# Kernel optimization log

Measured on AMD Instinct MI355X. Metric: run time of the kernel, lower is better.

Reference implementation:

```python
import jax, jax.numpy as jnp
import numpy as np

# dimensions
B, NQ, D, H, L, KT, KF = 4, 8192, 256, 8, 4, 2, 2
K = KT * KF
DH = D // H
SPATIAL = np.array([[64, 64], [32, 32], [16, 16], [8, 8]], dtype=np.int32)  # (H_l, W_l)
_sizes = SPATIAL[:, 0] * SPATIAL[:, 1]
LSI = np.concatenate([[0], np.cumsum(_sizes)[:-1]]).astype(np.int32)
NV = int(_sizes.sum())


def setup_inputs() -> dict:
    key = jax.random.key(0)
    ks = jax.random.split(key, 12)
    s = 0.02  # small weight scale keeps tanh in linear region like the zero-init original
    # biases per _reset_parameters: +-0.5 grid for offsets, level-specialization for level_weights
    b_time = jnp.asarray(np.tile(np.linspace(-0.5, 0.5, KT), H * L).astype(np.float32))
    b_freq = jnp.asarray(np.tile(np.linspace(-0.5, 0.5, KF).astype(np.float32), H * L))
    lvl_bias = np.zeros((H, L), dtype=np.float32)
    hpl = max(1, H // L)
    for lvl in range(L):
        lvl_bias[lvl * hpl:min(lvl * hpl + hpl, H), lvl] = 1.0
    return dict(
        query=jax.random.normal(ks[0], (B, NQ, D), jnp.float32),
        reference_points=jax.random.uniform(ks[1], (B, NQ, L, 2), jnp.float32),
        value=jax.random.normal(ks[2], (B, NV, D), jnp.float32),
        spatial_shapes=jnp.asarray(SPATIAL),
        level_start_index=jnp.asarray(LSI),
        W_time=jax.random.normal(ks[3], (D, H * L * KT), jnp.float32) * s,
        b_time=b_time,
        W_freq=jax.random.normal(ks[4], (D, H * L * KF), jnp.float32) * s,
        b_freq=b_freq,
        W_lvl=jax.random.normal(ks[5], (D, H * L), jnp.float32) * s,
        b_lvl=jnp.asarray(lvl_bias.reshape(-1)),
        W_pt=jax.random.normal(ks[6], (D, H * L * K), jnp.float32) * s,
        b_pt=jnp.zeros((H * L * K,), jnp.float32),
        W_v=jax.random.normal(ks[7], (D, D), jnp.float32) * (1.0 / np.sqrt(D)),
        b_v=jnp.zeros((D,), jnp.float32),
        W_o=jax.random.normal(ks[8], (D, D), jnp.float32) * (1.0 / np.sqrt(D)),
        b_o=jnp.zeros((D,), jnp.float32),
    )


def _bilinear(vlev, gx, gy, Hl, Wl):
    # vlev: [B,H,Hl*Wl,DH]; gx,gy: [B,H,NQ,K] normalized grid coords in [-1,1]
    # F.grid_sample(align_corners=False, padding_mode='zeros') semantics
    x = (gx + 1.0) * (Wl * 0.5) - 0.5
    y = (gy + 1.0) * (Hl * 0.5) - 0.5
    x0 = jnp.floor(x)
    y0 = jnp.floor(y)
    wx1 = x - x0
    wy1 = y - y0
    x0i = x0.astype(jnp.int32)
    y0i = y0.astype(jnp.int32)

    def gather(xi, yi, w):
        valid = (xi >= 0) & (xi < Wl) & (yi >= 0) & (yi < Hl)
        idx = jnp.clip(yi, 0, Hl - 1) * Wl + jnp.clip(xi, 0, Wl - 1)
        b, h, nq, k = idx.shape
        v = jnp.take_along_axis(vlev, idx.reshape(b, h, nq * k)[..., None], axis=2)
        v = v.reshape(b, h, nq, k, DH)
        return v * (w * valid)[..., None]

    return (gather(x0i, y0i, (1.0 - wx1) * (1.0 - wy1))
            + gather(x0i + 1, y0i, wx1 * (1.0 - wy1))
            + gather(x0i, y0i + 1, (1.0 - wx1) * wy1)
            + gather(x0i + 1, y0i + 1, wx1 * wy1))


def _forward(query, reference_points, value, W_time, b_time, W_freq, b_freq,
             W_lvl, b_lvl, W_pt, b_pt, W_v, b_v, W_o, b_o,
             spatial_shapes, level_start_index):
    ss = np.asarray(spatial_shapes)
    lsi = np.asarray(level_start_index)
    # predicted separable offsets (offset_scale = 1.0)
    t_off = jnp.tanh(query @ W_time + b_time).reshape(B, NQ, H, L, KT)
    f_off = jnp.tanh(query @ W_freq + b_freq).reshape(B, NQ, H, L, KF)
    # square grid: outer product of time (x) and freq (y) offsets -> K = KT*KF points
    off = jnp.stack([
        jnp.broadcast_to(t_off[..., :, None], (B, NQ, H, L, KT, KF)),
        jnp.broadcast_to(f_off[..., None, :], (B, NQ, H, L, KT, KF)),
    ], axis=-1).reshape(B, NQ, H, L, K, 2)
    # normalizer: (W_l, H_l) per level
    norm = jnp.stack([spatial_shapes[:, 1], spatial_shapes[:, 0]], axis=-1).astype(jnp.float32)
    loc = reference_points[:, :, None, :, None, :] + off / norm[None, None, None, :, None, :]
    loc = jnp.clip(loc, 0.0, 1.0)
    grid = 2.0 * loc - 1.0  # [B,NQ,H,L,K,2], last dim = (x, y)
    # attention weights: softmax over levels times softmax over points
    lw = jax.nn.softmax((query @ W_lvl + b_lvl).reshape(B, NQ, H, L), axis=-1)
    pw = jax.nn.softmax((query @ W_pt + b_pt).reshape(B, NQ, H, L, K), axis=-1)
    attn = lw[..., None] * pw  # [B,NQ,H,L,K]
    v = (value @ W_v + b_v).reshape(B, NV, H, DH)
    out = jnp.zeros((B, NQ, H, DH), jnp.float32)
    for lid in range(L):
        Hl, Wl = int(ss[lid, 0]), int(ss[lid, 1])
        start = int(lsi[lid])
        vlev = v[:, start:start + Hl * Wl].transpose(0, 2, 1, 3)  # [B,H,S_l,DH]
        gx = grid[:, :, :, lid, :, 0].transpose(0, 2, 1, 3)  # [B,H,NQ,K]
        gy = grid[:, :, :, lid, :, 1].transpose(0, 2, 1, 3)
        sampled = _bilinear(vlev, gx, gy, Hl, Wl)  # [B,H,NQ,K,DH]
        a = attn[:, :, :, lid, :].transpose(0, 2, 1, 3)  # [B,H,NQ,K]
        out = out + jnp.einsum('bhqkd,bhqk->bqhd', sampled, a)
    out = out.reshape(B, NQ, D)
    return out @ W_o + b_o


def reference(query, reference_points, value, spatial_shapes, level_start_index,
              W_time, b_time, W_freq, b_freq, W_lvl, b_lvl, W_pt, b_pt,
              W_v, b_v, W_o, b_o):
    return _forward(query, reference_points, value, W_time, b_time, W_freq, b_freq,
                    W_lvl, b_lvl, W_pt, b_pt, W_v, b_v, W_o, b_o,
                    spatial_shapes, level_start_index)
```

## Files before the change

### kernel.cpp

```cpp
#include <hip/hip_runtime.h>
#include <math.h>

#define B_  4
#define NQ_ 8192
#define D_  256
#define H_  8
#define L_  4
#define K_  4
#define DH_ 32
#define NV_ 5440

#define SLAB_ 5936

typedef short bf16x8 __attribute__((ext_vector_type(8)));
typedef float f32x4  __attribute__((ext_vector_type(4)));
typedef unsigned short u16x8 __attribute__((ext_vector_type(8)));

__device__ __forceinline__ ushort f2bf(float f) {
    union { float f; unsigned u; } v; v.f = f;
    return (ushort)((v.u + 0x7FFF + ((v.u >> 16) & 1)) >> 16);
}
__device__ __forceinline__ float bf2f(ushort u) {
    union { unsigned u; float f; } v; v.u = ((unsigned)u) << 16;
    return v.f;
}

__global__ __launch_bounds__(256) void k_zero(uint4* __restrict__ p) {
    p[(size_t)blockIdx.x * 256 + threadIdx.x] = make_uint4(0, 0, 0, 0);
}

__global__ __launch_bounds__(256) void k_cvta(const float* __restrict__ in,
                                              ushort* __restrict__ out) {
    const size_t base = ((size_t)blockIdx.x * 256 + threadIdx.x) * 8;
    const float4 a = *(const float4*)(in + base);
    const float4 b = *(const float4*)(in + base + 4);
    u16x8 u;
    u[0] = f2bf(a.x); u[1] = f2bf(a.y); u[2] = f2bf(a.z); u[3] = f2bf(a.w);
    u[4] = f2bf(b.x); u[5] = f2bf(b.y); u[6] = f2bf(b.z); u[7] = f2bf(b.w);
    *(u16x8*)(out + base) = u;
}

__global__ __launch_bounds__(256) void k_cvtw(const float* __restrict__ in,
                                              ushort* __restrict__ out) {
    const int n = blockIdx.x, k = threadIdx.x;
    out[n * 256 + k] = f2bf(in[k * 256 + n]);
}

__global__ __launch_bounds__(256) void k_cvtwq(const float* __restrict__ Wt,
                                               const float* __restrict__ Wf,
                                               const float* __restrict__ Wlv,
                                               const float* __restrict__ Wp,
                                               ushort* __restrict__ out) {
    const int n = blockIdx.x, k = threadIdx.x;
    float v;
    if (n < 64)       v = Wt[k * 64 + n];
    else if (n < 128) v = Wf[k * 64 + (n - 64)];
    else if (n < 160) v = Wlv[k * 32 + (n - 128)];
    else              v = Wp[k * 128 + (n - 160)];
    out[n * 256 + k] = f2bf(v);
}

template<int NT, int MODE, int AF32>
__global__ __launch_bounds__(256) void k_gemm(const void* __restrict__ Ap,
                                              const ushort* __restrict__ Bt,
                                              const float* __restrict__ bias,
                                              void* __restrict__ Cp) {
    constexpr int NFN = NT / 32;
    __shared__ ushort As[128 * 32];
    __shared__ ushort Bs[NT * 32];
    const int m0   = blockIdx.x * 128;
    const int n0   = blockIdx.y * NT;
    const int t    = threadIdx.x;
    const int w    = t >> 6;
    const int lane = t & 63;
    const int wm   = (w >> 1) * 64;
    const int wn   = (w & 1) * (NT / 2);
    const int lm   = lane & 15;
    const int quad = lane >> 4;

    f32x4 acc[4][NFN];
    #pragma unroll
    for (int i = 0; i < 4; ++i)
        #pragma unroll
        for (int j = 0; j < NFN; ++j)
            acc[i][j] = (f32x4)(0.f);

    for (int kc = 0; kc < 256; kc += 32) {
        __syncthreads();
        if (AF32) {
            const float* A = (const float*)Ap;
            #pragma unroll
            for (int i = 0; i < 4; ++i) {
                const int c   = t + i * 256;
                const int row = c >> 3, ko = (c & 7) * 4;
                const float4 v = *(const float4*)&A[(size_t)(m0 + row) * 256 + kc + ko];
                ushort4 u; u.x = f2bf(v.x); u.y = f2bf(v.y); u.z = f2bf(v.z); u.w = f2bf(v.w);
                *(ushort4*)&As[row * 32 + ko] = u;
            }
        } else {
            const ushort* A = (const ushort*)Ap;
            #pragma unroll
            for (int i = 0; i < 2; ++i) {
                const int c   = t + i * 256;
                const int row = c >> 2, ko = (c & 3) * 8;
                *(u16x8*)&As[row * 32 + ko] =
                    *(const u16x8*)&A[(size_t)(m0 + row) * 256 + kc + ko];
            }
        }
        #pragma unroll
        for (int i = 0; i < 2; ++i) {
            const int c = t + i * 256;
            if (NT == 128 || c < NT * 4) {
                const int row = c >> 2, ko = (c & 3) * 8;
                *(u16x8*)&Bs[row * 32 + ko] =
                    *(const u16x8*)&Bt[(size_t)(n0 + row) * 256 + kc + ko];
            }
        }
        __syncthreads();

        bf16x8 af[4], bfr[NFN];
        #pragma unroll
        for (int mf = 0; mf < 4; ++mf)
            af[mf] = *(const bf16x8*)&As[(wm + mf * 16 + lm) * 32 + quad * 8];
        #pragma unroll
        for (int nf = 0; nf < NFN; ++nf)
            bfr[nf] = *(const bf16x8*)&Bs[(wn + nf * 16 + lm) * 32 + quad * 8];
        #pragma unroll
        for (int mf = 0; mf < 4; ++mf)
            #pragma unroll
            for (int nf = 0; nf < NFN; ++nf)
                acc[mf][nf] = __builtin_amdgcn_mfma_f32_16x16x32_bf16(
                    af[mf], bfr[nf], acc[mf][nf], 0, 0, 0);
    }

    #pragma unroll
    for (int mf = 0; mf < 4; ++mf) {
        #pragma unroll
        for (int nf = 0; nf < NFN; ++nf) {
            const f32x4 a = acc[mf][nf];
            const int col   = n0 + wn + nf * 16 + lm;
            const int rbase = m0 + wm + mf * 16 + quad * 4;
            #pragma unroll
            for (int r = 0; r < 4; ++r) {
                const int row = rbase + r;
                const float v = a[r];
                if (MODE == 0) {
                    ((float*)Cp)[(size_t)row * 256 + col] = v + bias[col];
                } else if (MODE == 1) {
                    const int b = row / NV_, s = row - b * NV_;
                    const int h = col >> 5, dh = col & 31;
                    const int l = (s >= 5376) ? 3 : (s >= 5120) ? 2 : (s >= 4096) ? 1 : 0;
                    const int lsi_[4] = {0, 4096, 5120, 5376};
                    const int po_[4]  = {0, 4356, 5512, 5836};
                    const int o  = s - lsi_[l];
                    const int Wl = 64 >> l;
                    const int y  = o >> (6 - l);
                    const int x  = o & (Wl - 1);
                    const int prow = po_[l] + (y + 1) * (Wl + 2) + (x + 1);
                    ((ushort*)Cp)[(((size_t)(b * H_ + h)) * SLAB_ + prow) * 32 + dh] =
                        f2bf(v + bias[col]);
                } else {
                    ((float*)Cp)[(size_t)row * 288 + col] = v;
                }
            }
        }
    }
}

__global__ __launch_bounds__(256) void k_epi(const float* __restrict__ logits,
                                             const float* __restrict__ refpts,
                                             const float* __restrict__ bt,
                                             const float* __restrict__ bfq,
                                             const float* __restrict__ blv,
                                             const float* __restrict__ bp,
                                             float* __restrict__ params) {
    const int item = blockIdx.x * 256 + threadIdx.x;
    const int qg = item >> 5;
    const int hl = item & 31;
    const int h = hl >> 2, l = hl & 3;
    const float* lgr = logits + (size_t)qg * 288;

    const float tA = tanhf(lgr[hl * 2 + 0] + bt[hl * 2 + 0]);
    const float tB = tanhf(lgr[hl * 2 + 1] + bt[hl * 2 + 1]);
    const float fA = tanhf(lgr[64 + hl * 2 + 0] + bfq[hl * 2 + 0]);
    const float fB = tanhf(lgr[64 + hl * 2 + 1] + bfq[hl * 2 + 1]);

    const float l0 = lgr[128 + h * 4 + 0] + blv[h * 4 + 0];
    const float l1 = lgr[128 + h * 4 + 1] + blv[h * 4 + 1];
    const float l2 = lgr[128 + h * 4 + 2] + blv[h * 4 + 2];
    const float l3 = lgr[128 + h * 4 + 3] + blv[h * 4 + 3];
    const float lm = fmaxf(fmaxf(l0, l1), fmaxf(l2, l3));
    const float e0 = __expf(l0 - lm), e1 = __expf(l1 - lm);
    const float e2 = __expf(l2 - lm), e3 = __expf(l3 - lm);
    const float lsum = e0 + e1 + e2 + e3;
    const float lwv = ((l == 0) ? e0 : (l == 1) ? e1 : (l == 2) ? e2 : e3) / lsum;

    const float p0 = lgr[160 + hl * 4 + 0] + bp[hl * 4 + 0];
    const float p1 = lgr[160 + hl * 4 + 1] + bp[hl * 4 + 1];
    const float p2 = lgr[160 + hl * 4 + 2] + bp[hl * 4 + 2];
    const float p3 = lgr[160 + hl * 4 + 3] + bp[hl * 4 + 3];
    const float pmx = fmaxf(fmaxf(p0, p1), fmaxf(p2, p3));
    const float q0e = __expf(p0 - pmx), q1e = __expf(p1 - pmx);
    const float q2e = __expf(p2 - pmx), q3e = __expf(p3 - pmx);
    const float inv = lwv / (q0e + q1e + q2e + q3e);

    const float rx = refpts[((size_t)qg * L_ + l) * 2 + 0];
    const float ry = refpts[((size_t)qg * L_ + l) * 2 + 1];
    const float Wlf = (float)(64 >> l);
    const float Hlf = (float)(64 >> l);
    const float xA = fminf(fmaxf(rx + tA / Wlf, 0.f), 1.f) * Wlf - 0.5f;
    const float xB = fminf(fmaxf(rx + tB / Wlf, 0.f), 1.f) * Wlf - 0.5f;
    const float yA = fminf(fmaxf(ry + fA / Hlf, 0.f), 1.f) * Hlf - 0.5f;
    const float yB = fminf(fmaxf(ry + fB / Hlf, 0.f), 1.f) * Hlf - 0.5f;

    float* pp = params + (size_t)qg * 256 + hl * 8;
    pp[0] = q0e * inv; pp[1] = q1e * inv; pp[2] = q2e * inv; pp[3] = q3e * inv;
    pp[4] = xA; pp[5] = xB; pp[6] = yA; pp[7] = yB;
}

__global__ __launch_bounds__(256) void k_sample(const ushort* __restrict__ vperm,
                                                const float* __restrict__ params,
                                                ushort* __restrict__ mid) {
    __shared__ float pm[8][264];
    const int b   = blockIdx.y;
    const int q0  = blockIdx.x * 8;
    const int t   = threadIdx.x;
    const int qs  = t >> 6;
    const int sub = t & 63;
    const int h   = sub >> 3;
    const int dh4 = sub & 7;

    for (int i = t; i < 8 * 256; i += 256) {
        const int q = i >> 8, c = i & 255;
        pm[q][(c >> 5) * 33 + (c & 31)] = params[((size_t)(b * NQ_ + q0 + q)) * 256 + c];
    }
    __syncthreads();

    const ushort* vb = vperm + ((size_t)(b * H_ + h)) * SLAB_ * 32 + dh4 * 4;
    const int po_[4] = {0, 4356, 5512, 5836};

    #pragma unroll
    for (int i = 0; i < 2; ++i) {
        const int ql = qs + i * 4;
        f32x4 acc = (f32x4)(0.f);
        #pragma unroll
        for (int l = 0; l < L_; ++l) {
            const int W2 = (64 >> l) + 2;
            const ushort* vl = vb + (size_t)po_[l] * 32;
            const float* p  = &pm[ql][h * 33 + l * 8];
            const float a0 = p[0], a1 = p[1], a2 = p[2], a3 = p[3];
            const float xA = p[4], xB = p[5], yA = p[6], yB = p[7];
            const float xa0 = floorf(xA), xb0 = floorf(xB);
            const float ya0 = floorf(yA), yb0 = floorf(yB);
            const float fxa = xA - xa0, fxb = xB - xb0;
            const float fya = yA - ya0, fyb = yB - yb0;
            const int pxa = (int)xa0 + 1, pxb = (int)xb0 + 1;
            const int pya = (int)ya0 + 1, pyb = (int)yb0 + 1;
            #pragma unroll
            for (int k = 0; k < 4; ++k) {
                const int   px = (k & 2) ? pxb : pxa;
                const int   py = (k & 1) ? pyb : pya;
                const float fx = (k & 2) ? fxb : fxa;
                const float fy = (k & 1) ? fyb : fya;
                const float ak = (k == 0) ? a0 : (k == 1) ? a1 : (k == 2) ? a2 : a3;
                const ushort* c = vl + (size_t)(py * W2 + px) * 32;
                const ushort4 u00 = *(const ushort4*)c;
                const ushort4 u10 = *(const ushort4*)(c + 32);
                const ushort4 u01 = *(const ushort4*)(c + W2 * 32);
                const ushort4 u11 = *(const ushort4*)(c + (W2 + 1) * 32);
                const float gx = 1.f - fx, gy = 1.f - fy;
                const float w00 = ak * gx * gy, w10 = ak * fx * gy;
                const float w01 = ak * gx * fy, w11 = ak * fx * fy;
                f32x4 v;
                v.x = bf2f(u00.x) * w00 + bf2f(u10.x) * w10 + bf2f(u01.x) * w01 + bf2f(u11.x) * w11;
                v.y = bf2f(u00.y) * w00 + bf2f(u10.y) * w10 + bf2f(u01.y) * w01 + bf2f(u11.y) * w11;
                v.z = bf2f(u00.z) * w00 + bf2f(u10.z) * w10 + bf2f(u01.z) * w01 + bf2f(u11.z) * w11;
                v.w = bf2f(u00.w) * w00 + bf2f(u10.w) * w10 + bf2f(u01.w) * w01 + bf2f(u11.w) * w11;
                acc += v;
            }
        }
        ushort4 o;
        o.x = f2bf(acc.x); o.y = f2bf(acc.y); o.z = f2bf(acc.z); o.w = f2bf(acc.w);
        *(ushort4*)&mid[((size_t)(b * NQ_ + q0 + ql)) * 256 + sub * 4] = o;
    }
}

extern "C" void kernel_launch(void* const* d_in, const int* in_sizes, int n_in,
                              void* d_out, int out_size, void* d_ws, size_t ws_size,
                              hipStream_t stream) {
    const float* query = (const float*)d_in[0];
    const float* refp  = (const float*)d_in[1];
    const float* value = (const float*)d_in[2];
    const float* Wt = (const float*)d_in[5];
    const float* bt = (const float*)d_in[6];
    const float* Wf = (const float*)d_in[7];
    const float* bf = (const float*)d_in[8];
    const float* Wl = (const float*)d_in[9];
    const float* bl = (const float*)d_in[10];
    const float* Wp = (const float*)d_in[11];
    const float* bp = (const float*)d_in[12];
    const float* Wv = (const float*)d_in[13];
    const float* bv = (const float*)d_in[14];
    const float* Wo = (const float*)d_in[15];
    const float* bo = (const float*)d_in[16];

    char* wsb = (char*)d_ws;
    ushort* vperm  = (ushort*)wsb;
    float*  params = (float*)(wsb + 12156928);
    ushort* qbf    = (ushort*)(wsb + 12156928);
    float*  logits = (float*)(wsb + 45711360);
    ushort* midb   = (ushort*)(wsb + 45711360);
    ushort* Wvt    = (ushort*)(wsb + 83460096);
    ushort* Wot    = (ushort*)(wsb + 83591168);
    ushort* Wqt    = (ushort*)(wsb + 83722240);

    k_cvtw<<<256, 256, 0, stream>>>(Wv, Wvt);
    k_cvtw<<<256, 256, 0, stream>>>(Wo, Wot);
    k_cvtwq<<<288, 256, 0, stream>>>(Wt, Wf, Wl, Wp, Wqt);
    k_cvta<<<4096, 256, 0, stream>>>(query, qbf);
    k_zero<<<2968, 256, 0, stream>>>((uint4*)vperm);

    k_gemm<128, 1, 1><<<dim3(170, 2), 256, 0, stream>>>(value, Wvt, bv, vperm);
    k_gemm<96, 2, 0><<<dim3(256, 3), 256, 0, stream>>>(qbf, Wqt, nullptr, logits);
    k_epi<<<4096, 256, 0, stream>>>(logits, refp, bt, bf, bl, bp, params);
    k_sample<<<dim3(NQ_ / 8, B_), 256, 0, stream>>>(vperm, params, midb);
    k_gemm<128, 0, 0><<<dim3(256, 2), 256, 0, stream>>>(midb, Wot, bo, (float*)d_out);
}
```

Measured before the change: 260.4 us.

## Fuse prep kernels, use direct global-to-LDS loads, stage GEMM epilogue, widen sampling

Five small conversion and zeroing launches become one k_prep kernel, which now also converts value to bf16 so the value GEMM reads bf16. GEMM tile loads use global_load_lds to skip the register round trip. The GEMM epilogue goes through shared memory so each thread writes vector rows instead of scattered scalars. The sampler gives each thread 8 channels of one query instead of 4 channels of two queries, for wider loads. The cost is an extra bf16 value buffer and more barriers in the epilogue.

```diff
diff --git a/kernel.cpp b/kernel.cpp
--- a/kernel.cpp
+++ b/kernel.cpp
@@ -14,7 +14,11 @@
 
 typedef short bf16x8 __attribute__((ext_vector_type(8)));
 typedef float f32x4  __attribute__((ext_vector_type(4)));
+typedef float f32x8  __attribute__((ext_vector_type(8)));
 typedef unsigned short u16x8 __attribute__((ext_vector_type(8)));
+
+typedef __attribute__((address_space(3))) ushort lds_ushort;
+typedef const __attribute__((address_space(1))) ushort glb_ushort;
 
 __device__ __forceinline__ ushort f2bf(float f) {
     union { float f; unsigned u; } v; v.f = f;
@@ -24,50 +28,72 @@
     union { unsigned u; float f; } v; v.u = ((unsigned)u) << 16;
     return v.f;
 }
-
-__global__ __launch_bounds__(256) void k_zero(uint4* __restrict__ p) {
-    p[(size_t)blockIdx.x * 256 + threadIdx.x] = make_uint4(0, 0, 0, 0);
-}
-
-__global__ __launch_bounds__(256) void k_cvta(const float* __restrict__ in,
-                                              ushort* __restrict__ out) {
-    const size_t base = ((size_t)blockIdx.x * 256 + threadIdx.x) * 8;
-    const float4 a = *(const float4*)(in + base);
-    const float4 b = *(const float4*)(in + base + 4);
-    u16x8 u;
-    u[0] = f2bf(a.x); u[1] = f2bf(a.y); u[2] = f2bf(a.z); u[3] = f2bf(a.w);
-    u[4] = f2bf(b.x); u[5] = f2bf(b.y); u[6] = f2bf(b.z); u[7] = f2bf(b.w);
-    *(u16x8*)(out + base) = u;
-}
-
-__global__ __launch_bounds__(256) void k_cvtw(const float* __restrict__ in,
-                                              ushort* __restrict__ out) {
-    const int n = blockIdx.x, k = threadIdx.x;
-    out[n * 256 + k] = f2bf(in[k * 256 + n]);
-}
-
-__global__ __launch_bounds__(256) void k_cvtwq(const float* __restrict__ Wt,
-                                               const float* __restrict__ Wf,
-                                               const float* __restrict__ Wlv,
-                                               const float* __restrict__ Wp,
-                                               ushort* __restrict__ out) {
-    const int n = blockIdx.x, k = threadIdx.x;
-    float v;
-    if (n < 64)       v = Wt[k * 64 + n];
-    else if (n < 128) v = Wf[k * 64 + (n - 64)];
-    else if (n < 160) v = Wlv[k * 32 + (n - 128)];
-    else              v = Wp[k * 128 + (n - 160)];
-    out[n * 256 + k] = f2bf(v);
-}
-
-template<int NT, int MODE, int AF32>
-__global__ __launch_bounds__(256) void k_gemm(const void* __restrict__ Ap,
+__device__ __forceinline__ void gload_lds16(const ushort* g, ushort* l) {
+    __builtin_amdgcn_global_load_lds((glb_ushort*)(unsigned long long)g,
+                                     (lds_ushort*)(unsigned)(unsigned long long)l,
+                                     16, 0, 0);
+}
+
+__global__ __launch_bounds__(256) void k_prep(const float* __restrict__ query,
+                                              const float* __restrict__ value,
+                                              const float* __restrict__ Wv,
+                                              const float* __restrict__ Wo,
+                                              const float* __restrict__ Wt,
+                                              const float* __restrict__ Wf,
+                                              const float* __restrict__ Wlv,
+                                              const float* __restrict__ Wp,
+                                              ushort* __restrict__ qbf,
+                                              ushort* __restrict__ valbf,
+                                              uint4* __restrict__ vzero,
+                                              ushort* __restrict__ Wvt,
+                                              ushort* __restrict__ Wot,
+                                              ushort* __restrict__ Wqt) {
+    const int bk = blockIdx.x;
+    const int t  = threadIdx.x;
+    if (bk < 6816) {
+        const float* in; ushort* out; int blk;
+        if (bk < 4096) { in = query; out = qbf; blk = bk; }
+        else           { in = value; out = valbf; blk = bk - 4096; }
+        const size_t base = ((size_t)blk * 256 + t) * 8;
+        const float4 a = *(const float4*)(in + base);
+        const float4 b = *(const float4*)(in + base + 4);
+        u16x8 u;
+        u[0] = f2bf(a.x); u[1] = f2bf(a.y); u[2] = f2bf(a.z); u[3] = f2bf(a.w);
+        u[4] = f2bf(b.x); u[5] = f2bf(b.y); u[6] = f2bf(b.z); u[7] = f2bf(b.w);
+        *(u16x8*)(out + base) = u;
+    } else if (bk < 9784) {
+        vzero[(size_t)(bk - 6816) * 256 + t] = make_uint4(0, 0, 0, 0);
+    } else if (bk < 10296) {
+        const float* in; ushort* out; int n;
+        if (bk < 10040) { in = Wv; out = Wvt; n = bk - 9784; }
+        else            { in = Wo; out = Wot; n = bk - 10040; }
+        out[n * 256 + t] = f2bf(in[t * 256 + n]);
+    } else {
+        const int n = bk - 10296;
+        float v;
+        if (n < 64)       v = Wt[t * 64 + n];
+        else if (n < 128) v = Wf[t * 64 + (n - 64)];
+        else if (n < 160) v = Wlv[t * 32 + (n - 128)];
+        else              v = Wp[t * 128 + (n - 160)];
+        Wqt[n * 256 + t] = f2bf(v);
+    }
+}
+
+template<int NT, int MODE>
+__global__ __launch_bounds__(256) void k_gemm(const ushort* __restrict__ A,
                                               const ushort* __restrict__ Bt,
                                               const float* __restrict__ bias,
                                               void* __restrict__ Cp) {
-    constexpr int NFN = NT / 32;
-    __shared__ ushort As[128 * 32];
-    __shared__ ushort Bs[NT * 32];
+    constexpr int NFN  = NT / 32;
+    constexpr int SW   = NT + 4;
+    constexpr int SSTG = (128 * 32 + NT * 32) * 2;
+    constexpr int SEPI = 32 * SW * 4;
+    constexpr int SMEM = (SSTG > SEPI) ? SSTG : SEPI;
+    __shared__ __align__(16) char smem[SMEM];
+    ushort* As  = (ushort*)smem;
+    ushort* Bs  = As + 128 * 32;
+    float*  sep = (float*)smem;
+
     const int m0   = blockIdx.x * 128;
     const int n0   = blockIdx.y * NT;
     const int t    = threadIdx.x;
@@ -87,34 +113,18 @@
 
     for (int kc = 0; kc < 256; kc += 32) {
         __syncthreads();
-        if (AF32) {
-            const float* A = (const float*)Ap;
-            #pragma unroll
-            for (int i = 0; i < 4; ++i) {
-                const int c   = t + i * 256;
-                const int row = c >> 3, ko = (c & 7) * 4;
-                const float4 v = *(const float4*)&A[(size_t)(m0 + row) * 256 + kc + ko];
-                ushort4 u; u.x = f2bf(v.x); u.y = f2bf(v.y); u.z = f2bf(v.z); u.w = f2bf(v.w);
-                *(ushort4*)&As[row * 32 + ko] = u;
-            }
-        } else {
-            const ushort* A = (const ushort*)Ap;
-            #pragma unroll
-            for (int i = 0; i < 2; ++i) {
-                const int c   = t + i * 256;
-                const int row = c >> 2, ko = (c & 3) * 8;
-                *(u16x8*)&As[row * 32 + ko] =
-                    *(const u16x8*)&A[(size_t)(m0 + row) * 256 + kc + ko];
-            }
+        #pragma unroll
+        for (int i = 0; i < 4; ++i) {
+            const int c = t + i * 256;
+            gload_lds16(&A[(size_t)(m0 + (c >> 2)) * 256 + kc + (c & 3) * 8],
+                        &As[c * 8]);
         }
         #pragma unroll
         for (int i = 0; i < 2; ++i) {
             const int c = t + i * 256;
-            if (NT == 128 || c < NT * 4) {
-                const int row = c >> 2, ko = (c & 3) * 8;
-                *(u16x8*)&Bs[row * 32 + ko] =
-                    *(const u16x8*)&Bt[(size_t)(n0 + row) * 256 + kc + ko];
-            }
+            if (NT == 128 || c < NT * 4)
+                gload_lds16(&Bt[(size_t)(n0 + (c >> 2)) * 256 + kc + (c & 3) * 8],
+                            &Bs[c * 8]);
         }
         __syncthreads();
 
@@ -133,35 +143,60 @@
                     af[mf], bfr[nf], acc[mf][nf], 0, 0, 0);
     }
 
+    const int lr0 = (w >> 1) * 16;
     #pragma unroll
     for (int mf = 0; mf < 4; ++mf) {
-        #pragma unroll
-        for (int nf = 0; nf < NFN; ++nf) {
-            const f32x4 a = acc[mf][nf];
-            const int col   = n0 + wn + nf * 16 + lm;
-            const int rbase = m0 + wm + mf * 16 + quad * 4;
-            #pragma unroll
-            for (int r = 0; r < 4; ++r) {
-                const int row = rbase + r;
-                const float v = a[r];
-                if (MODE == 0) {
-                    ((float*)Cp)[(size_t)row * 256 + col] = v + bias[col];
-                } else if (MODE == 1) {
-                    const int b = row / NV_, s = row - b * NV_;
-                    const int h = col >> 5, dh = col & 31;
-                    const int l = (s >= 5376) ? 3 : (s >= 5120) ? 2 : (s >= 4096) ? 1 : 0;
-                    const int lsi_[4] = {0, 4096, 5120, 5376};
-                    const int po_[4]  = {0, 4356, 5512, 5836};
-                    const int o  = s - lsi_[l];
-                    const int Wl = 64 >> l;
-                    const int y  = o >> (6 - l);
-                    const int x  = o & (Wl - 1);
-                    const int prow = po_[l] + (y + 1) * (Wl + 2) + (x + 1);
-                    ((ushort*)Cp)[(((size_t)(b * H_ + h)) * SLAB_ + prow) * 32 + dh] =
-                        f2bf(v + bias[col]);
-                } else {
-                    ((float*)Cp)[(size_t)row * 288 + col] = v;
+        __syncthreads();
+        #pragma unroll
+        for (int nf = 0; nf < NFN; ++nf)
+            #pragma unroll
+            for (int r = 0; r < 4; ++r)
+                sep[(lr0 + quad * 4 + r) * SW + wn + nf * 16 + lm] = acc[mf][nf][r];
+        __syncthreads();
+
+        const int lr   = t >> 3;
+        const int band = lr >> 4, ri = lr & 15;
+        const int gr   = m0 + band * 64 + mf * 16 + ri;
+        const int c0   = (t & 7) * (NT / 8);
+
+        if (MODE == 0) {
+            float* C = (float*)Cp;
+            #pragma unroll
+            for (int j = 0; j < NT / 32; ++j) {
+                f32x4 v = *(f32x4*)&sep[lr * SW + c0 + j * 4];
+                const int col = n0 + c0 + j * 4;
+                v.x += bias[col]; v.y += bias[col + 1];
+                v.z += bias[col + 2]; v.w += bias[col + 3];
+                *(f32x4*)&C[(size_t)gr * 256 + col] = v;
+            }
+        } else if (MODE == 2) {
+            float* C = (float*)Cp;
+            #pragma unroll
+            for (int j = 0; j < NT / 32; ++j)
+                *(f32x4*)&C[(size_t)gr * 288 + n0 + c0 + j * 4] =
+                    *(f32x4*)&sep[lr * SW + c0 + j * 4];
+        } else {
+            const int b = gr / NV_, s = gr - b * NV_;
+            const int l = (s >= 5376) ? 3 : (s >= 5120) ? 2 : (s >= 4096) ? 1 : 0;
+            const int lsi_[4] = {0, 4096, 5120, 5376};
+            const int po_[4]  = {0, 4356, 5512, 5836};
+            const int o  = s - lsi_[l];
+            const int Wl = 64 >> l;
+            const int y  = o >> (6 - l);
+            const int x  = o & (Wl - 1);
+            const int prow = po_[l] + (y + 1) * (Wl + 2) + (x + 1);
+            const int h   = (n0 + c0) >> 5;
+            const int dh0 = (n0 + c0) & 31;
+            ushort* dst = (ushort*)Cp + (((size_t)(b * H_ + h)) * SLAB_ + prow) * 32 + dh0;
+            #pragma unroll
+            for (int j2 = 0; j2 < 2; ++j2) {
+                u16x8 u;
+                #pragma unroll
+                for (int e = 0; e < 8; ++e) {
+                    const int cc = c0 + j2 * 8 + e;
+                    u[e] = f2bf(sep[lr * SW + cc] + bias[n0 + cc]);
                 }
+                *(u16x8*)(dst + j2 * 8) = u;
             }
         }
     }
@@ -225,10 +260,10 @@
     const int b   = blockIdx.y;
     const int q0  = blockIdx.x * 8;
     const int t   = threadIdx.x;
-    const int qs  = t >> 6;
-    const int sub = t & 63;
-    const int h   = sub >> 3;
-    const int dh4 = sub & 7;
+    const int ql  = t >> 5;
+    const int sub = t & 31;
+    const int h   = sub >> 2;
+    const int dh8 = sub & 3;
 
     for (int i = t; i < 8 * 256; i += 256) {
         const int q = i >> 8, c = i & 255;
@@ -236,53 +271,48 @@
     }
     __syncthreads();
 
-    const ushort* vb = vperm + ((size_t)(b * H_ + h)) * SLAB_ * 32 + dh4 * 4;
+    const ushort* vb = vperm + ((size_t)(b * H_ + h)) * SLAB_ * 32 + dh8 * 8;
     const int po_[4] = {0, 4356, 5512, 5836};
 
+    f32x8 acc = (f32x8)(0.f);
     #pragma unroll
-    for (int i = 0; i < 2; ++i) {
-        const int ql = qs + i * 4;
-        f32x4 acc = (f32x4)(0.f);
-        #pragma unroll
-        for (int l = 0; l < L_; ++l) {
-            const int W2 = (64 >> l) + 2;
-            const ushort* vl = vb + (size_t)po_[l] * 32;
-            const float* p  = &pm[ql][h * 33 + l * 8];
-            const float a0 = p[0], a1 = p[1], a2 = p[2], a3 = p[3];
-            const float xA = p[4], xB = p[5], yA = p[6], yB = p[7];
-            const float xa0 = floorf(xA), xb0 = floorf(xB);
-            const float ya0 = floorf(yA), yb0 = floorf(yB);
-            const float fxa = xA - xa0, fxb = xB - xb0;
-            const float fya = yA - ya0, fyb = yB - yb0;
-            const int pxa = (int)xa0 + 1, pxb = (int)xb0 + 1;
-            const int pya = (int)ya0 + 1, pyb = (int)yb0 + 1;
-            #pragma unroll
-            for (int k = 0; k < 4; ++k) {
-                const int   px = (k & 2) ? pxb : pxa;
-                const int   py = (k & 1) ? pyb : pya;
-                const float fx = (k & 2) ? fxb : fxa;
-                const float fy = (k & 1) ? fyb : fya;
-                const float ak = (k == 0) ? a0 : (k == 1) ? a1 : (k == 2) ? a2 : a3;
-                const ushort* c = vl + (size_t)(py * W2 + px) * 32;
-                const ushort4 u00 = *(const ushort4*)c;
-                const ushort4 u10 = *(const ushort4*)(c + 32);
-                const ushort4 u01 = *(const ushort4*)(c + W2 * 32);
-                const ushort4 u11 = *(const ushort4*)(c + (W2 + 1) * 32);
-                const float gx = 1.f - fx, gy = 1.f - fy;
-                const float w00 = ak * gx * gy, w10 = ak * fx * gy;
-                const float w01 = ak * gx * fy, w11 = ak * fx * fy;
-                f32x4 v;
-                v.x = bf2f(u00.x) * w00 + bf2f(u10.x) * w10 + bf2f(u01.x) * w01 + bf2f(u11.x) * w11;
-                v.y = bf2f(u00.y) * w00 + bf2f(u10.y) * w10 + bf2f(u01.y) * w01 + bf2f(u11.y) * w11;
-                v.z = bf2f(u00.z) * w00 + bf2f(u10.z) * w10 + bf2f(u01.z) * w01 + bf2f(u11.z) * w11;
-                v.w = bf2f(u00.w) * w00 + bf2f(u10.w) * w10 + bf2f(u01.w) * w01 + bf2f(u11.w) * w11;
-                acc += v;
-            }
+    for (int l = 0; l < L_; ++l) {
+        const int W2 = (64 >> l) + 2;
+        const ushort* vl = vb + (size_t)po_[l] * 32;
+        const float* p  = &pm[ql][h * 33 + l * 8];
+        const float a0 = p[0], a1 = p[1], a2 = p[2], a3 = p[3];
+        const float xA = p[4], xB = p[5], yA = p[6], yB = p[7];
+        const float xa0 = floorf(xA), xb0 = floorf(xB);
+        const float ya0 = floorf(yA), yb0 = floorf(yB);
+        const float fxa = xA - xa0, fxb = xB - xb0;
+        const float fya = yA - ya0, fyb = yB - yb0;
+        const int pxa = (int)xa0 + 1, pxb = (int)xb0 + 1;
+        const int pya = (int)ya0 + 1, pyb = (int)yb0 + 1;
+        #pragma unroll
+        for (int k = 0; k < 4; ++k) {
+            const int   px = (k & 2) ? pxb : pxa;
+            const int   py = (k & 1) ? pyb : pya;
+            const float fx = (k & 2) ? fxb : fxa;
+            const float fy = (k & 1) ? fyb : fya;
+            const float ak = (k == 0) ? a0 : (k == 1) ? a1 : (k == 2) ? a2 : a3;
+            const ushort* cp = vl + (size_t)(py * W2 + px) * 32;
+            const u16x8 u00 = *(const u16x8*)cp;
+            const u16x8 u10 = *(const u16x8*)(cp + 32);
+            const u16x8 u01 = *(const u16x8*)(cp + W2 * 32);
+            const u16x8 u11 = *(const u16x8*)(cp + (W2 + 1) * 32);
+            const float gx = 1.f - fx, gy = 1.f - fy;
+            const float w00 = ak * gx * gy, w10 = ak * fx * gy;
+            const float w01 = ak * gx * fy, w11 = ak * fx * fy;
+            #pragma unroll
+            for (int e = 0; e < 8; ++e)
+                acc[e] += bf2f(u00[e]) * w00 + bf2f(u10[e]) * w10
+                        + bf2f(u01[e]) * w01 + bf2f(u11[e]) * w11;
         }
-        ushort4 o;
-        o.x = f2bf(acc.x); o.y = f2bf(acc.y); o.z = f2bf(acc.z); o.w = f2bf(acc.w);
-        *(ushort4*)&mid[((size_t)(b * NQ_ + q0 + ql)) * 256 + sub * 4] = o;
-    }
+    }
+    u16x8 o;
+    #pragma unroll
+    for (int e = 0; e < 8; ++e) o[e] = f2bf(acc[e]);
+    *(u16x8*)&mid[((size_t)(b * NQ_ + q0 + ql)) * 256 + sub * 8] = o;
 }
 
 extern "C" void kernel_launch(void* const* d_in, const int* in_sizes, int n_in,
@@ -310,19 +340,16 @@
     ushort* qbf    = (ushort*)(wsb + 12156928);
     float*  logits = (float*)(wsb + 45711360);
     ushort* midb   = (ushort*)(wsb + 45711360);
-    ushort* Wvt    = (ushort*)(wsb + 83460096);
-    ushort* Wot    = (ushort*)(wsb + 83591168);
-    ushort* Wqt    = (ushort*)(wsb + 83722240);
-
-    k_cvtw<<<256, 256, 0, stream>>>(Wv, Wvt);
-    k_cvtw<<<256, 256, 0, stream>>>(Wo, Wot);
-    k_cvtwq<<<288, 256, 0, stream>>>(Wt, Wf, Wl, Wp, Wqt);
-    k_cvta<<<4096, 256, 0, stream>>>(query, qbf);
-    k_zero<<<2968, 256, 0, stream>>>((uint4*)vperm);
-
-    k_gemm<128, 1, 1><<<dim3(170, 2), 256, 0, stream>>>(value, Wvt, bv, vperm);
-    k_gemm<96, 2, 0><<<dim3(256, 3), 256, 0, stream>>>(qbf, Wqt, nullptr, logits);
+    ushort* valbf  = (ushort*)(wsb + 83460096);
+    ushort* Wvt    = (ushort*)(wsb + 94601216);
+    ushort* Wot    = (ushort*)(wsb + 94732288);
+    ushort* Wqt    = (ushort*)(wsb + 94863360);
+
+    k_prep<<<10584, 256, 0, stream>>>(query, value, Wv, Wo, Wt, Wf, Wl, Wp,
+                                      qbf, valbf, (uint4*)vperm, Wvt, Wot, Wqt);
+    k_gemm<128, 1><<<dim3(170, 2), 256, 0, stream>>>(valbf, Wvt, bv, vperm);
+    k_gemm<96, 2><<<dim3(256, 3), 256, 0, stream>>>(qbf, Wqt, nullptr, logits);
     k_epi<<<4096, 256, 0, stream>>>(logits, refp, bt, bf, bl, bp, params);
     k_sample<<<dim3(NQ_ / 8, B_), 256, 0, stream>>>(vperm, params, midb);
-    k_gemm<128, 0, 0><<<dim3(256, 2), 256, 0, stream>>>(midb, Wot, bo, (float*)d_out);
-}
+    k_gemm<128, 0><<<dim3(256, 2), 256, 0, stream>>>(midb, Wot, bo, (float*)d_out);
+}
```

Result: no change. 262.6 us (+0.8%).
